# Kernel optimization log

Hardware: AMD Instinct MI355X
Metric: run time of the kernel (lower is better)

## Reference

```python
import jax, jax.numpy as jnp
import numpy as np

N = 50000      # nodes
E = 1600000    # edges (avg degree 32)
D = 64         # d_node
DE = 32        # d_edge
H = 4          # heads
L = 3          # layers


def _ln(x, g, b):
    mu = x.mean(-1, keepdims=True)
    var = ((x - mu) ** 2).mean(-1, keepdims=True)
    return (x - mu) / jnp.sqrt(var + 1e-5) * g + b


def setup_inputs() -> dict:
    key = jax.random.key(0)
    ks = jax.random.split(key, 16)
    s = 0.05
    return {
        "node_features": jax.random.normal(ks[0], (N, D), jnp.float32),
        "edge_features": jax.random.normal(ks[1], (E, DE), jnp.float32),
        "edge_index": jax.random.randint(ks[2], (2, E), 0, N),
        "Wq": jax.random.normal(ks[3], (L, D, D), jnp.float32) * s,
        "Wk": jax.random.normal(ks[4], (L, D, D), jnp.float32) * s,
        "Wv": jax.random.normal(ks[5], (L, D, D), jnp.float32) * s,
        "Wo": jax.random.normal(ks[6], (L, D, D), jnp.float32) * s,
        "We": jax.random.normal(ks[7], (L, DE, H), jnp.float32) * s,   # edge-conditioned score bias
        "Wem": jax.random.normal(ks[8], (L, 2 * D + DE, DE), jnp.float32) * s,
        "bem": jnp.zeros((L, DE), jnp.float32),
        "gn": jnp.ones((L, D), jnp.float32),
        "bn": jnp.zeros((L, D), jnp.float32),
        "ge": jnp.ones((L, DE), jnp.float32),
        "be": jnp.zeros((L, DE), jnp.float32),
    }


def _delta_forward(h, e, src, dst, Wq, Wk, Wv, Wo, We, Wem, bem, gn, bn, ge, be):
    n = h.shape[0]
    dh = D // H
    for i in range(L):
        # --- node attention over edges (sparse, per-dst segment softmax) ---
        q = (h @ Wq[i]).reshape(n, H, dh)
        k = (h @ Wk[i]).reshape(n, H, dh)
        v = (h @ Wv[i]).reshape(n, H, dh)
        scores = jnp.einsum('ehd,ehd->eh', q[dst], k[src]) / jnp.sqrt(jnp.float32(dh))
        scores = scores + e @ We[i]                         # edge-conditioned bias [E,H]
        m = jax.ops.segment_max(scores, dst, num_segments=n)
        p = jnp.exp(scores - m[dst])
        denom = jax.ops.segment_sum(p, dst, num_segments=n)
        alpha = p / (denom[dst] + 1e-9)                      # [E,H]
        msg = (alpha[:, :, None] * v[src]).reshape(-1, D)    # [E,D]
        agg = jax.ops.segment_sum(msg, dst, num_segments=n)  # [N,D]
        h = _ln(h + agg @ Wo[i], gn[i], bn[i])
        # --- edge update conditioned on endpoint nodes ---
        emsg = jax.nn.gelu(jnp.concatenate([h[src], h[dst], e], axis=-1) @ Wem[i] + bem[i])
        e = _ln(e + emsg, ge[i], be[i])
    return h


def reference(node_features, edge_features, edge_index, Wq, Wk, Wv, Wo, We, Wem, bem, gn, bn, ge, be):
    src = edge_index[0]
    dst = edge_index[1]
    return _delta_forward(node_features, edge_features, src, dst,
                          Wq, Wk, Wv, Wo, We, Wem, bem, gn, bn, ge, be)
```

## Files before the change

### kernel.cpp

```cpp
#include <hip/hip_runtime.h>
#include <hip/hip_bf16.h>
#include <math.h>

#define NN 50000
#define NE 1600000
#define D 64
#define DE 32
#define H 4
#define DH 16
#define L 3

typedef __attribute__((ext_vector_type(8))) short bf16x8;
typedef __attribute__((ext_vector_type(8))) short s16x8;
typedef __attribute__((ext_vector_type(4))) float f32x4;
typedef __attribute__((ext_vector_type(4))) unsigned int u32x4;

__device__ __forceinline__ short f2b(float f) {
    __hip_bfloat16 h = __float2bfloat16(f);
    short s;
    __builtin_memcpy(&s, &h, 2);
    return s;
}
__device__ __forceinline__ float b2f(unsigned short u) {
    unsigned int x = ((unsigned int)u) << 16;
    float f; __builtin_memcpy(&f, &x, 4); return f;
}
__device__ __forceinline__ float b2f_lo(unsigned int p) {
    unsigned int x = p << 16;
    float f; __builtin_memcpy(&f, &x, 4); return f;
}
__device__ __forceinline__ float b2f_hi(unsigned int p) {
    unsigned int x = p & 0xffff0000u;
    float f; __builtin_memcpy(&f, &x, 4); return f;
}


__global__ void deg_kernel(const int* __restrict__ dst, int* __restrict__ cnt) {
    int e = blockIdx.x * 256 + threadIdx.x;
    if (e >= NE) return;
    atomicAdd(&cnt[dst[e]], 1);
}

__global__ void block_sum_kernel(const int* __restrict__ cnt, int* __restrict__ bsum) {
    int b = blockIdx.x, t = threadIdx.x;
    int base = b * 1024 + t * 4;
    int s = 0;
#pragma unroll
    for (int i = 0; i < 4; i++) { int idx = base + i; if (idx < NN) s += cnt[idx]; }
#pragma unroll
    for (int off = 32; off; off >>= 1) s += __shfl_down(s, off);
    __shared__ int wsum[4];
    if ((t & 63) == 0) wsum[t >> 6] = s;
    __syncthreads();
    if (t == 0) bsum[b] = wsum[0] + wsum[1] + wsum[2] + wsum[3];
}

__global__ void scan_bsum_kernel(int* __restrict__ bsum, int nb) {
    int t = threadIdx.x;
    int v = (t < nb) ? bsum[t] : 0;
    int x = v;
#pragma unroll
    for (int off = 1; off < 64; off <<= 1) {
        int y = __shfl_up(x, off);
        if (t >= off) x += y;
    }
    if (t < nb) bsum[t] = x - v;
}

__global__ void scan_block_kernel(int* __restrict__ cnt, const int* __restrict__ bsum,
                                  int* __restrict__ offsets) {
    int b = blockIdx.x, t = threadIdx.x;
    int base = b * 1024 + t * 4;
    int v[4]; int s = 0;
#pragma unroll
    for (int i = 0; i < 4; i++) { int idx = base + i; v[i] = (idx < NN) ? cnt[idx] : 0; s += v[i]; }
    int lane = t & 63, w = t >> 6;
    int x = s;
#pragma unroll
    for (int off = 1; off < 64; off <<= 1) {
        int y = __shfl_up(x, off);
        if (lane >= off) x += y;
    }
    __shared__ int wsum[4];
    if (lane == 63) wsum[w] = x;
    __syncthreads();
    int woff = 0;
    for (int i = 0; i < w; i++) woff += wsum[i];
    int run = bsum[b] + woff + x - s;
#pragma unroll
    for (int i = 0; i < 4; i++) {
        int idx = base + i;
        if (idx < NN) { offsets[idx] = run; cnt[idx] = run; }
        run += v[i];
    }
}

__global__ void scatter_kernel(const int* __restrict__ src, const int* __restrict__ dst,
                               int* __restrict__ cursor,
                               int2* __restrict__ sorted_es) {
    int e = blockIdx.x * 256 + threadIdx.x;
    if (e >= NE) return;
    int d0 = dst[e];
    int pos = atomicAdd(&cursor[d0], 1);
    int2 v; v.x = e; v.y = src[e];
    sorted_es[pos] = v;
}

__global__ void fill_dst_kernel(const int* __restrict__ offsets, int* __restrict__ sorted_dst) {
    int n = blockIdx.x * 256 + threadIdx.x;
    if (n >= NN) return;
    int b = offsets[n];
    int e = (n == NN - 1) ? NE : offsets[n + 1];
    for (int i = b; i < e; i++) sorted_dst[i] = n;
}

__global__ void eperm_kernel(const float* __restrict__ e32, const int2* __restrict__ sorted_es,
                             const float* __restrict__ We0,
                             unsigned short* __restrict__ eb_s,
                             float* __restrict__ ebias_s) {
    int t = blockIdx.x * 256 + threadIdx.x;
    if (t >= NE * 4) return;
    int p = t >> 2;
    int c = (t & 3) * 8;
    int eid = sorted_es[p].x;
    const float* ep = e32 + (size_t)eid * DE + c;
    float4 x0 = *(const float4*)(ep);
    float4 x1 = *(const float4*)(ep + 4);
    float e8[8] = {x0.x, x0.y, x0.z, x0.w, x1.x, x1.y, x1.z, x1.w};
    s16x8 ob;
#pragma unroll
    for (int i = 0; i < 8; i++) ob[i] = f2b(e8[i]);
    *(s16x8*)(eb_s + (size_t)p * DE + c) = ob;
    float p0 = 0.f, p1 = 0.f, p2 = 0.f, p3 = 0.f;
#pragma unroll
    for (int i = 0; i < 8; i++) {
        float4 w = *(const float4*)(We0 + (c + i) * 4);
        p0 += e8[i] * w.x; p1 += e8[i] * w.y; p2 += e8[i] * w.z; p3 += e8[i] * w.w;
    }
#pragma unroll
    for (int off = 1; off < 4; off <<= 1) {
        p0 += __shfl_xor(p0, off, 4);
        p1 += __shfl_xor(p1, off, 4);
        p2 += __shfl_xor(p2, off, 4);
        p3 += __shfl_xor(p3, off, 4);
    }
    if ((t & 3) == 0) {
        float4 o; o.x = p0; o.y = p1; o.z = p2; o.w = p3;
        *(float4*)(ebias_s + (size_t)p * H) = o;
    }
}

__global__ void wconv_kernel(const float* __restrict__ Wem, unsigned short* __restrict__ Wt) {
    int t = blockIdx.x * 256 + threadIdx.x;
    if (t >= L * 32 * 160) return;
    int l = t / 5120;
    int r = t % 5120;
    int n = r / 160;
    int k = r % 160;
    Wt[t] = (unsigned short)f2b(Wem[l * 5120 + k * 32 + n]);
}

__global__ void wsplit_kernel(const float* __restrict__ Wq, const float* __restrict__ Wk,
                              const float* __restrict__ Wv, const float* __restrict__ Wo,
                              unsigned short* __restrict__ WT_hi,
                              unsigned short* __restrict__ WT_lo) {
    int t = blockIdx.x * 256 + threadIdx.x;
    if (t >= L * 4 * 64 * 64) return;
    int k = t & 63;
    int n = (t >> 6) & 63;
    int mat = (t >> 12) & 3;
    int l = t >> 14;
    const float* W = (mat == 0) ? Wq : (mat == 1) ? Wk : (mat == 2) ? Wv : Wo;
    float w = W[l * 4096 + k * 64 + n];
    unsigned short hi = (unsigned short)f2b(w);
    float lo = w - b2f(hi);
    WT_hi[t] = hi;
    WT_lo[t] = (unsigned short)f2b(lo);
}

__global__ void hconv_kernel(const float* __restrict__ nf, float* __restrict__ h,
                             unsigned short* __restrict__ hb) {
    int t = blockIdx.x * 256 + threadIdx.x;
    if (t >= NN * D) return;
    float x = nf[t];
    h[t] = x;
    hb[t] = (unsigned short)f2b(x);
}


__global__ __launch_bounds__(256, 8)
void qkv_kernel(const float* __restrict__ h,
                const unsigned short* __restrict__ WT_hi,
                const unsigned short* __restrict__ WT_lo,
                float* __restrict__ q, unsigned int* __restrict__ kv) {
    int lane = threadIdx.x & 63;
    int wv = threadIdx.x >> 6;
    int m = lane & 15, quad = lane >> 4;
    int base = blockIdx.x * 16;

    const float* hp = h + (size_t)(base + m) * D + quad * 8;
    float af[16];
    *(f32x4*)&af[0]  = *(const f32x4*)(hp);
    *(f32x4*)&af[4]  = *(const f32x4*)(hp + 4);
    *(f32x4*)&af[8]  = *(const f32x4*)(hp + 32);
    *(f32x4*)&af[12] = *(const f32x4*)(hp + 36);
    bf16x8 a0h, a0l, a1h, a1l;
#pragma unroll
    for (int j = 0; j < 8; j++) {
        short h0 = f2b(af[j]);
        short h1 = f2b(af[8 + j]);
        a0h[j] = h0; a0l[j] = f2b(af[j] - b2f((unsigned short)h0));
        a1h[j] = h1; a1l[j] = f2b(af[8 + j] - b2f((unsigned short)h1));
    }

    f32x4 acc[3];
#pragma unroll
    for (int mat = 0; mat < 3; mat++) {
        const unsigned short* bh = WT_hi + ((size_t)mat * 64 + wv * 16 + m) * 64 + quad * 8;
        const unsigned short* bl = WT_lo + ((size_t)mat * 64 + wv * 16 + m) * 64 + quad * 8;
        bf16x8 bh0 = *(const bf16x8*)(bh);
        bf16x8 bh1 = *(const bf16x8*)(bh + 32);
        bf16x8 bl0 = *(const bf16x8*)(bl);
        bf16x8 bl1 = *(const bf16x8*)(bl + 32);
        f32x4 c = {0.f, 0.f, 0.f, 0.f};
        c = __builtin_amdgcn_mfma_f32_16x16x32_bf16(a0h, bh0, c, 0, 0, 0);
        c = __builtin_amdgcn_mfma_f32_16x16x32_bf16(a1h, bh1, c, 0, 0, 0);
        c = __builtin_amdgcn_mfma_f32_16x16x32_bf16(a0h, bl0, c, 0, 0, 0);
        c = __builtin_amdgcn_mfma_f32_16x16x32_bf16(a1h, bl1, c, 0, 0, 0);
        c = __builtin_amdgcn_mfma_f32_16x16x32_bf16(a0l, bh0, c, 0, 0, 0);
        c = __builtin_amdgcn_mfma_f32_16x16x32_bf16(a1l, bh1, c, 0, 0, 0);
        acc[mat] = c;
    }

#pragma unroll
    for (int reg = 0; reg < 4; reg++) {
        int row = base + quad * 4 + reg;
        int col = wv * 16 + m;
        q[(size_t)row * D + col] = acc[0][reg] * 0.25f;
        unsigned int kb = (unsigned short)f2b(acc[1][reg]);
        unsigned int vb = (unsigned short)f2b(acc[2][reg]);
        kv[(size_t)row * D + col] = (vb << 16) | kb;
    }
}

__global__ __launch_bounds__(256, 8)
void attn_kernel(const float* __restrict__ q, const unsigned int* __restrict__ kv,
                 const float* __restrict__ ebias_s,
                 const int2* __restrict__ es,
                 const int* __restrict__ offsets,
                 float* __restrict__ agg) {
    __shared__ __align__(16) float sacc[4][4][16][20];
    int wave = threadIdx.y;
    int node = blockIdx.x * 4 + wave;
    node = __builtin_amdgcn_readfirstlane(node);
    if (node >= NN) return;
    int lane = threadIdx.x;
    int u = lane & 15, hh = lane >> 4;

    float qv[16];
    const float* qp = q + (size_t)node * D + hh * 16;
    *(f32x4*)&qv[0]  = *(const f32x4*)(qp);
    *(f32x4*)&qv[4]  = *(const f32x4*)(qp + 4);
    *(f32x4*)&qv[8]  = *(const f32x4*)(qp + 8);
    *(f32x4*)&qv[12] = *(const f32x4*)(qp + 12);

    int beg = offsets[node];
    int end = (node == NN - 1) ? NE : offsets[node + 1];
    float den = 0.f;
    float acc[16];
#pragma unroll
    for (int j = 0; j < 16; j++) acc[j] = 0.f;

    for (int i = beg; i < end; i += 16) {
        int idx = i + u;
        bool valid = idx < end;
        int sidx = valid ? idx : (end - 1);
        int s = es[sidx].y;
        float bias = ebias_s[sidx * H + hh];
        const unsigned int* kp = kv + (size_t)s * D + hh * 16;
        unsigned int kr[16];
        *(u32x4*)&kr[0]  = *(const u32x4*)(kp);
        *(u32x4*)&kr[4]  = *(const u32x4*)(kp + 4);
        *(u32x4*)&kr[8]  = *(const u32x4*)(kp + 8);
        *(u32x4*)&kr[12] = *(const u32x4*)(kp + 12);
        float dot = bias;
#pragma unroll
        for (int j = 0; j < 16; j++) dot += qv[j] * b2f_lo(kr[j]);
        float p = valid ? __expf(dot) : 0.f;
        den += p;
#pragma unroll
        for (int j = 0; j < 16; j++) acc[j] += p * b2f_hi(kr[j]);
    }

    *(f32x4*)&sacc[wave][hh][u][0]  = *(const f32x4*)&acc[0];
    *(f32x4*)&sacc[wave][hh][u][4]  = *(const f32x4*)&acc[4];
    *(f32x4*)&sacc[wave][hh][u][8]  = *(const f32x4*)&acc[8];
    *(f32x4*)&sacc[wave][hh][u][12] = *(const f32x4*)&acc[12];
#pragma unroll
    for (int off = 1; off < 16; off <<= 1) den += __shfl_xor(den, off, 16);
    float o = 0.f;
#pragma unroll
    for (int u2 = 0; u2 < 16; u2++) o += sacc[wave][hh][u2][u];
    agg[(size_t)node * D + hh * 16 + u] = o / (den + 1e-9f);
}

__global__ __launch_bounds__(256, 8)
void node_update_kernel(float* __restrict__ h, const float* __restrict__ agg,
                        const unsigned short* __restrict__ WoT_hi,
                        const unsigned short* __restrict__ WoT_lo,
                        const float* __restrict__ gn,
                        const float* __restrict__ bn,
                        unsigned short* __restrict__ hb) {
    __shared__ float sx[16][68];
    int lane = threadIdx.x & 63;
    int wv = threadIdx.x >> 6;
    int m = lane & 15, quad = lane >> 4;
    int base = blockIdx.x * 16;

    const float* ap = agg + (size_t)(base + m) * D + quad * 8;
    float af[16];
    *(f32x4*)&af[0]  = *(const f32x4*)(ap);
    *(f32x4*)&af[4]  = *(const f32x4*)(ap + 4);
    *(f32x4*)&af[8]  = *(const f32x4*)(ap + 32);
    *(f32x4*)&af[12] = *(const f32x4*)(ap + 36);
    bf16x8 a0h, a0l, a1h, a1l;
#pragma unroll
    for (int j = 0; j < 8; j++) {
        short h0 = f2b(af[j]);
        short h1 = f2b(af[8 + j]);
        a0h[j] = h0; a0l[j] = f2b(af[j] - b2f((unsigned short)h0));
        a1h[j] = h1; a1l[j] = f2b(af[8 + j] - b2f((unsigned short)h1));
    }
    const unsigned short* bh = WoT_hi + ((size_t)wv * 16 + m) * 64 + quad * 8;
    const unsigned short* bl = WoT_lo + ((size_t)wv * 16 + m) * 64 + quad * 8;
    bf16x8 bh0 = *(const bf16x8*)(bh);
    bf16x8 bh1 = *(const bf16x8*)(bh + 32);
    bf16x8 bl0 = *(const bf16x8*)(bl);
    bf16x8 bl1 = *(const bf16x8*)(bl + 32);
    f32x4 c = {0.f, 0.f, 0.f, 0.f};
    c = __builtin_amdgcn_mfma_f32_16x16x32_bf16(a0h, bh0, c, 0, 0, 0);
    c = __builtin_amdgcn_mfma_f32_16x16x32_bf16(a1h, bh1, c, 0, 0, 0);
    c = __builtin_amdgcn_mfma_f32_16x16x32_bf16(a0h, bl0, c, 0, 0, 0);
    c = __builtin_amdgcn_mfma_f32_16x16x32_bf16(a1h, bl1, c, 0, 0, 0);
    c = __builtin_amdgcn_mfma_f32_16x16x32_bf16(a0l, bh0, c, 0, 0, 0);
    c = __builtin_amdgcn_mfma_f32_16x16x32_bf16(a1l, bh1, c, 0, 0, 0);

#pragma unroll
    for (int reg = 0; reg < 4; reg++) {
        int row = quad * 4 + reg;
        int col = wv * 16 + m;
        sx[row][col] = c[reg] + h[(size_t)(base + row) * D + col];
    }
    __syncthreads();

    float gcol = gn[lane], bcol = bn[lane];
#pragma unroll
    for (int it = 0; it < 4; it++) {
        int ln = wv * 4 + it;
        int node = base + ln;
        float x = sx[ln][lane];
        float sum = x, sq = x * x;
#pragma unroll
        for (int off = 32; off; off >>= 1) {
            sum += __shfl_xor(sum, off);
            sq += __shfl_xor(sq, off);
        }
        float mu = sum * (1.f / 64.f);
        float var = sq * (1.f / 64.f) - mu * mu;
        float out = (x - mu) * rsqrtf(var + 1e-5f) * gcol + bcol;
        h[(size_t)node * D + lane] = out;
        hb[(size_t)node * D + lane] = (unsigned short)f2b(out);
    }
}

__global__ __launch_bounds__(256, 4)
void edge_update_mfma_kernel(const unsigned short* __restrict__ hb,
                             unsigned short* __restrict__ eb_s,
                             const int2* __restrict__ es,
                             const int* __restrict__ sorted_dst,
                             const unsigned short* __restrict__ Wt,
                             const float* __restrict__ bem,
                             const float* __restrict__ ge,
                             const float* __restrict__ be,
                             const float* __restrict__ We_next,
                             float* __restrict__ ebias_s,
                             int do_bias, int do_estore) {
    __shared__ __align__(16) float ytr[4][16][36];
    int tid = threadIdx.x;
    int wave = tid >> 6;
    int lane = tid & 63;
    int wbase = blockIdx.x * 256 + wave * 64;
    int m = lane & 15;
    int quad = lane >> 4;

    const unsigned short* w0 = Wt + m * 160 + quad * 8;
    const unsigned short* w1 = Wt + (m + 16) * 160 + quad * 8;
    bf16x8 B0[5], B1[5];
#pragma unroll
    for (int ks = 0; ks < 5; ks++) {
        B0[ks] = *(const bf16x8*)(w0 + ks * 32);
        B1[ks] = *(const bf16x8*)(w1 + ks * 32);
    }
    bf16x8 wb;
#pragma unroll
    for (int j = 0; j < 8; j++) {
        float w = (do_bias && m < 4) ? We_next[(quad * 8 + j) * 4 + m] : 0.f;
        wb[j] = f2b(w);
    }
    float bm0 = bem[m], bm1 = bem[m + 16];
    float4 g0v = *(const float4*)(ge + quad * 8);
    float4 g1v = *(const float4*)(ge + quad * 8 + 4);
    float4 b0v = *(const float4*)(be + quad * 8);
    float4 b1v = *(const float4*)(be + quad * 8 + 4);
    float gg[8] = {g0v.x, g0v.y, g0v.z, g0v.w, g1v.x, g1v.y, g1v.z, g1v.w};
    float bbv[8] = {b0v.x, b0v.y, b0v.z, b0v.w, b1v.x, b1v.y, b1v.z, b1v.w};

    for (int g = 0; g < 4; g++) {
        int we = wbase + g * 16;
        int p_m = we + m;
        int s_idx = es[p_m].y, d_idx = sorted_dst[p_m];
        const unsigned short* as = hb + (size_t)s_idx * D + quad * 8;
        const unsigned short* ad = hb + (size_t)d_idx * D + quad * 8;
        bf16x8 a_s0 = *(const bf16x8*)(as);
        bf16x8 a_s1 = *(const bf16x8*)(as + 32);
        bf16x8 a_d0 = *(const bf16x8*)(ad);
        bf16x8 a_d1 = *(const bf16x8*)(ad + 32);
        bf16x8 ea = *(const bf16x8*)(eb_s + (size_t)p_m * DE + quad * 8);

        f32x4 c0 = {0.f, 0.f, 0.f, 0.f};
        f32x4 c1 = {0.f, 0.f, 0.f, 0.f};
#pragma unroll
        for (int ks = 0; ks < 4; ks++) {
            bf16x8 a = (ks == 0) ? a_s0 : (ks == 1) ? a_s1 : (ks == 2) ? a_d0 : a_d1;
            c0 = __builtin_amdgcn_mfma_f32_16x16x32_bf16(a, B0[ks], c0, 0, 0, 0);
            c1 = __builtin_amdgcn_mfma_f32_16x16x32_bf16(a, B1[ks], c1, 0, 0, 0);
        }
        c0 = __builtin_amdgcn_mfma_f32_16x16x32_bf16(ea, B0[4], c0, 0, 0, 0);
        c1 = __builtin_amdgcn_mfma_f32_16x16x32_bf16(ea, B1[4], c1, 0, 0, 0);

#pragma unroll
        for (int reg = 0; reg < 4; reg++) {
            int row = quad * 4 + reg;
            float y0 = c0[reg] + bm0;
            float y1 = c1[reg] + bm1;
            float u0 = 1.5957691216057308f * (y0 + 0.044715f * y0 * y0 * y0);
            float u1 = 1.5957691216057308f * (y1 + 0.044715f * y1 * y1 * y1);
            float t0 = 1.f - 2.f / (1.f + __expf(u0));
            float t1 = 1.f - 2.f / (1.f + __expf(u1));
            ytr[wave][row][m] = 0.5f * y0 * (1.f + t0);
            ytr[wave][row][m + 16] = 0.5f * y1 * (1.f + t1);
        }

        float y[8];
        *(f32x4*)&y[0] = *(const f32x4*)&ytr[wave][m][quad * 8];
        *(f32x4*)&y[4] = *(const f32x4*)&ytr[wave][m][quad * 8 + 4];
        float s = 0.f, sq = 0.f;
#pragma unroll
        for (int j = 0; j < 8; j++) {
            y[j] += b2f((unsigned short)ea[j]);
            s += y[j];
            sq += y[j] * y[j];
        }
        s += __shfl_xor(s, 16); s += __shfl_xor(s, 32);
        sq += __shfl_xor(sq, 16); sq += __shfl_xor(sq, 32);
        float mu = s * (1.f / 32.f);
        float var = sq * (1.f / 32.f) - mu * mu;
        float inv = rsqrtf(var + 1e-5f);

        bf16x8 zb;
#pragma unroll
        for (int j = 0; j < 8; j++) {
            float z = (y[j] - mu) * inv * gg[j] + bbv[j];
            zb[j] = f2b(z);
        }
        if (do_estore) {
            *(s16x8*)(eb_s + (size_t)p_m * DE + quad * 8) = zb;
        }
        if (do_bias) {
            f32x4 db = {0.f, 0.f, 0.f, 0.f};
            db = __builtin_amdgcn_mfma_f32_16x16x32_bf16(zb, wb, db, 0, 0, 0);
            if (m < 4) {
#pragma unroll
                for (int reg = 0; reg < 4; reg++) {
                    ebias_s[(we + quad * 4 + reg) * H + m] = db[reg];
                }
            }
        }
    }
}

extern "C" void kernel_launch(void* const* d_in, const int* in_sizes, int n_in,
                              void* d_out, int out_size, void* d_ws, size_t ws_size,
                              hipStream_t stream) {
    const float* node_features = (const float*)d_in[0];
    const float* e = (const float*)d_in[1];
    const int* edge_index = (const int*)d_in[2];
    const int* src = edge_index;
    const int* dst = edge_index + NE;
    const float* Wq = (const float*)d_in[3];
    const float* Wk = (const float*)d_in[4];
    const float* Wv = (const float*)d_in[5];
    const float* Wo = (const float*)d_in[6];
    const float* We = (const float*)d_in[7];
    const float* Wem = (const float*)d_in[8];
    const float* bem = (const float*)d_in[9];
    const float* gn = (const float*)d_in[10];
    const float* bn = (const float*)d_in[11];
    const float* ge = (const float*)d_in[12];
    const float* be = (const float*)d_in[13];

    float* h = (float*)d_out;

    float* ws = (float*)d_ws;
    float* q = ws;
    unsigned int* kv = (unsigned int*)(q + NN * D);
    float* agg = (float*)(kv + NN * D);
    float* ebias_s = agg + NN * D;
    int* offsets = (int*)(ebias_s + (size_t)NE * H);
    int* cursor = offsets + NN;
    int* bsum = cursor + NN;
    int2* sorted_es = (int2*)(bsum + 64);
    int* sorted_dst = (int*)(sorted_es + NE);
    unsigned short* Wt = (unsigned short*)(sorted_dst + NE);
    unsigned short* hb = Wt + L * 32 * 160;
    unsigned short* eb_s = hb + NN * D;
    unsigned short* WT_hi = eb_s + (size_t)NE * DE;
    unsigned short* WT_lo = WT_hi + L * 4 * 64 * 64;

    const int NB = (NN + 1023) / 1024;

    hipMemsetAsync(cursor, 0, NN * sizeof(int), stream);
    deg_kernel<<<(NE + 255) / 256, 256, 0, stream>>>(dst, cursor);
    block_sum_kernel<<<NB, 256, 0, stream>>>(cursor, bsum);
    scan_bsum_kernel<<<1, 64, 0, stream>>>(bsum, NB);
    scan_block_kernel<<<NB, 256, 0, stream>>>(cursor, bsum, offsets);
    scatter_kernel<<<(NE + 255) / 256, 256, 0, stream>>>(src, dst, cursor, sorted_es);
    fill_dst_kernel<<<(NN + 255) / 256, 256, 0, stream>>>(offsets, sorted_dst);
    eperm_kernel<<<(NE * 4 + 255) / 256, 256, 0, stream>>>(e, sorted_es, We, eb_s, ebias_s);
    wconv_kernel<<<(L * 32 * 160 + 255) / 256, 256, 0, stream>>>(Wem, Wt);
    wsplit_kernel<<<(L * 4 * 64 * 64 + 255) / 256, 256, 0, stream>>>(Wq, Wk, Wv, Wo,
                                                                     WT_hi, WT_lo);
    hconv_kernel<<<(NN * D + 255) / 256, 256, 0, stream>>>(node_features, h, hb);

    for (int layer = 0; layer < L; layer++) {
        const unsigned short* WT_hi_l = WT_hi + (size_t)layer * 4 * 4096;
        const unsigned short* WT_lo_l = WT_lo + (size_t)layer * 4 * 4096;
        const unsigned short* Wt_l = Wt + layer * 32 * 160;
        const float* bem_l = bem + layer * DE;
        const float* gn_l = gn + layer * D;
        const float* bn_l = bn + layer * D;
        const float* ge_l = ge + layer * DE;
        const float* be_l = be + layer * DE;

        qkv_kernel<<<NN / 16, 256, 0, stream>>>(h, WT_hi_l, WT_lo_l, q, kv);
        attn_kernel<<<NN / 4, dim3(64, 4), 0, stream>>>(q, kv, ebias_s, sorted_es,
                                                        offsets, agg);
        node_update_kernel<<<NN / 16, 256, 0, stream>>>(h, agg,
                                                        WT_hi_l + 3 * 4096,
                                                        WT_lo_l + 3 * 4096,
                                                        gn_l, bn_l, hb);
        if (layer < L - 1) {
            const float* We_next = We + (layer + 1) * DE * H;
            edge_update_mfma_kernel<<<NE / 256, 256, 0, stream>>>(hb, eb_s, sorted_es,
                                                                  sorted_dst, Wt_l,
                                                                  bem_l, ge_l, be_l,
                                                                  We_next, ebias_s,
                                                                  1, layer == 0 ? 1 : 0);
        }
    }
}
```

Baseline: 1.113 ms.

## Replace global-atomic CSR scatter with two-pass bucketed binning sort

Replaces the per-edge global atomicAdd scatter and the serial per-node fill of sorted_dst with a two-level counting sort. Edges are first binned by coarse dst bucket (1024 nodes) using shared-memory histograms and one global atomic per bucket per block. A second kernel then places edges within each bucket using shared-memory atomics and writes sorted_dst at the same time. The aim is to cut global atomic contention and the imbalanced fill loop, at the cost of an extra pass over a 16-byte-per-edge intermediate buffer and a fine pass that runs only 49 blocks.

```diff
diff --git a/kernel.cpp b/kernel.cpp
--- a/kernel.cpp
+++ b/kernel.cpp
@@ -9,6 +9,8 @@
 #define H 4
 #define DH 16
 #define L 3
+#define BKT_SHIFT 10
+#define NBKT 49
 
 typedef __attribute__((ext_vector_type(8))) short bf16x8;
 typedef __attribute__((ext_vector_type(8))) short s16x8;
@@ -67,7 +69,7 @@
     if (t < nb) bsum[t] = x - v;
 }
 
-__global__ void scan_block_kernel(int* __restrict__ cnt, const int* __restrict__ bsum,
+__global__ void scan_block_kernel(const int* __restrict__ cnt, const int* __restrict__ bsum,
                                   int* __restrict__ offsets) {
     int b = blockIdx.x, t = threadIdx.x;
     int base = b * 1024 + t * 4;
@@ -90,28 +92,67 @@
 #pragma unroll
     for (int i = 0; i < 4; i++) {
         int idx = base + i;
-        if (idx < NN) { offsets[idx] = run; cnt[idx] = run; }
+        if (idx < NN) offsets[idx] = run;
         run += v[i];
     }
 }
 
-__global__ void scatter_kernel(const int* __restrict__ src, const int* __restrict__ dst,
-                               int* __restrict__ cursor,
-                               int2* __restrict__ sorted_es) {
-    int e = blockIdx.x * 256 + threadIdx.x;
-    if (e >= NE) return;
-    int d0 = dst[e];
-    int pos = atomicAdd(&cursor[d0], 1);
-    int2 v; v.x = e; v.y = src[e];
-    sorted_es[pos] = v;
-}
-
-__global__ void fill_dst_kernel(const int* __restrict__ offsets, int* __restrict__ sorted_dst) {
-    int n = blockIdx.x * 256 + threadIdx.x;
-    if (n >= NN) return;
-    int b = offsets[n];
-    int e = (n == NN - 1) ? NE : offsets[n + 1];
-    for (int i = b; i < e; i++) sorted_dst[i] = n;
+__global__ void init_bkt_kernel(const int* __restrict__ offsets, int* __restrict__ bucket_cursor) {
+    int t = threadIdx.x;
+    if (t < NBKT) bucket_cursor[t] = offsets[t << BKT_SHIFT];
+}
+
+__global__ __launch_bounds__(256)
+void bin_kernel(const int* __restrict__ src, const int* __restrict__ dst,
+                int* __restrict__ bucket_cursor, int4* __restrict__ binned) {
+    __shared__ int hist[64], base[64];
+    int tid = threadIdx.x;
+    if (tid < 64) hist[tid] = 0;
+    __syncthreads();
+    int e0 = blockIdx.x * 1024;
+    int ee[4], s4[4], d4[4], bk[4], rk[4];
+#pragma unroll
+    for (int i = 0; i < 4; i++) {
+        int e = e0 + tid + i * 256;
+        ee[i] = e;
+        bool v = e < NE;
+        d4[i] = v ? dst[e] : 0;
+        s4[i] = v ? src[e] : 0;
+        bk[i] = d4[i] >> BKT_SHIFT;
+        rk[i] = v ? atomicAdd(&hist[bk[i]], 1) : 0;
+    }
+    __syncthreads();
+    if (tid < 64) base[tid] = hist[tid] ? atomicAdd(&bucket_cursor[tid], hist[tid]) : 0;
+    __syncthreads();
+#pragma unroll
+    for (int i = 0; i < 4; i++) {
+        if (ee[i] < NE) {
+            int4 v; v.x = ee[i]; v.y = s4[i]; v.z = d4[i]; v.w = 0;
+            binned[base[bk[i]] + rk[i]] = v;
+        }
+    }
+}
+
+__global__ __launch_bounds__(1024)
+void fine_scatter_kernel(const int4* __restrict__ binned, const int* __restrict__ offsets,
+                         int2* __restrict__ sorted_es, int* __restrict__ sorted_dst) {
+    __shared__ int cur[1024];
+    int b = blockIdx.x;
+    int nbase = b << BKT_SHIFT;
+    int tid = threadIdx.x;
+    int nid = nbase + tid;
+    cur[tid] = (nid < NN) ? offsets[nid] : 0;
+    int beg = offsets[nbase];
+    int nend = nbase + 1024;
+    int end = (nend >= NN) ? NE : offsets[nend];
+    __syncthreads();
+    for (int i = beg + tid; i < end; i += 1024) {
+        int4 v = binned[i];
+        int pos = atomicAdd(&cur[v.z - nbase], 1);
+        int2 es; es.x = v.x; es.y = v.y;
+        sorted_es[pos] = es;
+        sorted_dst[pos] = v.z;
+    }
 }
 
 __global__ void eperm_kernel(const float* __restrict__ e32, const int2* __restrict__ sorted_es,
@@ -519,9 +560,11 @@
     int* offsets = (int*)(ebias_s + (size_t)NE * H);
     int* cursor = offsets + NN;
     int* bsum = cursor + NN;
-    int2* sorted_es = (int2*)(bsum + 64);
+    int* bucket_cursor = bsum + 64;
+    int2* sorted_es = (int2*)(bucket_cursor + 64);
     int* sorted_dst = (int*)(sorted_es + NE);
-    unsigned short* Wt = (unsigned short*)(sorted_dst + NE);
+    int4* binned = (int4*)(sorted_dst + NE);
+    unsigned short* Wt = (unsigned short*)(binned + NE);
     unsigned short* hb = Wt + L * 32 * 160;
     unsigned short* eb_s = hb + NN * D;
     unsigned short* WT_hi = eb_s + (size_t)NE * DE;
@@ -534,8 +577,9 @@
     block_sum_kernel<<<NB, 256, 0, stream>>>(cursor, bsum);
     scan_bsum_kernel<<<1, 64, 0, stream>>>(bsum, NB);
     scan_block_kernel<<<NB, 256, 0, stream>>>(cursor, bsum, offsets);
-    scatter_kernel<<<(NE + 255) / 256, 256, 0, stream>>>(src, dst, cursor, sorted_es);
-    fill_dst_kernel<<<(NN + 255) / 256, 256, 0, stream>>>(offsets, sorted_dst);
+    init_bkt_kernel<<<1, 64, 0, stream>>>(offsets, bucket_cursor);
+    bin_kernel<<<(NE + 1023) / 1024, 256, 0, stream>>>(src, dst, bucket_cursor, binned);
+    fine_scatter_kernel<<<NBKT, 1024, 0, stream>>>(binned, offsets, sorted_es, sorted_dst);
     eperm_kernel<<<(NE * 4 + 255) / 256, 256, 0, stream>>>(e, sorted_es, We, eb_s, ebias_s);
     wconv_kernel<<<(L * 32 * 160 + 255) / 256, 256, 0, stream>>>(Wem, Wt);
     wsplit_kernel<<<(L * 4 * 64 * 64 + 255) / 256, 256, 0, stream>>>(Wq, Wk, Wv, Wo,
```

Measured after the change: 1.078 ms. 3.1% less time.
